# Performance work log

Hardware: AMD Instinct MI355X
Metric: run time of the kernel (lower is better)

Reference implementation:

```python
import jax, jax.numpy as jnp
import numpy as np

N, E, G = 40000, 400000, 64
IN, ED, HID, HEADS, OUT = 2, 18, 64, 4, 3

def _glorot(key, shape):
    fan_in = shape[0]
    return jax.random.normal(key, shape, dtype=jnp.float32) / np.float32(np.sqrt(fan_in))

def setup_inputs():
    key = jax.random.key(0)
    ks = jax.random.split(key, 32)
    d1 = HEADS * HID  # 256
    return {
        "x": jax.random.normal(ks[0], (N, IN), jnp.float32),
        "edge_index": jax.random.randint(ks[1], (2, E), 0, N),
        "edge_attr": jax.random.normal(ks[2], (E, ED), jnp.float32),
        "batch": jnp.sort(jax.random.randint(ks[3], (N,), 0, G)),
        # conv1: TransformerConv(2 -> 64, heads=4, concat=True, beta=True, edge_dim=18)
        "Wq1": _glorot(ks[4], (IN, d1)), "bq1": jnp.zeros((d1,), jnp.float32),
        "Wk1": _glorot(ks[5], (IN, d1)), "bk1": jnp.zeros((d1,), jnp.float32),
        "Wv1": _glorot(ks[6], (IN, d1)), "bv1": jnp.zeros((d1,), jnp.float32),
        "We1": _glorot(ks[7], (ED, d1)),
        "Wskip1": _glorot(ks[8], (IN, d1)), "bskip1": jnp.zeros((d1,), jnp.float32),
        "Wbeta1": _glorot(ks[9], (3 * d1, 1)),
        # conv2: TransformerConv(256 -> 64, heads=1, concat=False, beta=True, edge_dim=18)
        "Wq2": _glorot(ks[10], (d1, HID)), "bq2": jnp.zeros((HID,), jnp.float32),
        "Wk2": _glorot(ks[11], (d1, HID)), "bk2": jnp.zeros((HID,), jnp.float32),
        "Wv2": _glorot(ks[12], (d1, HID)), "bv2": jnp.zeros((HID,), jnp.float32),
        "We2": _glorot(ks[13], (ED, HID)),
        "Wskip2": _glorot(ks[14], (d1, HID)), "bskip2": jnp.zeros((HID,), jnp.float32),
        "Wbeta2": _glorot(ks[15], (3 * HID, 1)),
        "Wlin": _glorot(ks[16], (HID, OUT)), "blin": jnp.zeros((OUT,), jnp.float32),
    }

def _tconv(x, src, dst, edge_attr, Wq, bq, Wk, bk, Wv, bv, We, Wskip, bskip, Wbeta, H, C, concat):
    # PyG TransformerConv with edge_dim, beta=True, root_weight=True (eval: dropout off)
    n = x.shape[0]
    q = (x @ Wq + bq).reshape(n, H, C)
    k = (x @ Wk + bk).reshape(n, H, C)
    v = (x @ Wv + bv).reshape(n, H, C)
    e = (edge_attr @ We).reshape(-1, H, C)              # [E,H,C]
    kj = k[src] + e                                      # key_j + edge
    alpha = jnp.einsum('ehc,ehc->eh', q[dst], kj) * (1.0 / (C ** 0.5))  # [E,H]
    # segment softmax over destination nodes
    amax = jax.ops.segment_max(alpha, dst, num_segments=n)
    ex = jnp.exp(alpha - amax[dst])
    den = jax.ops.segment_sum(ex, dst, num_segments=n)
    w = ex / (den[dst] + 1e-16)
    msg = (v[src] + e) * w[:, :, None]                   # [E,H,C]
    out = jax.ops.segment_sum(msg, dst, num_segments=n)  # [N,H,C]
    out = out.reshape(n, H * C) if concat else out.mean(axis=1)
    # beta-gated skip connection
    xr = x @ Wskip + bskip
    beta = jax.nn.sigmoid(jnp.concatenate([out, xr, out - xr], axis=-1) @ Wbeta)
    return beta * xr + (1.0 - beta) * out

def reference(x, edge_index, edge_attr, batch, Wq1, bq1, Wk1, bk1, Wv1, bv1, We1, Wskip1, bskip1, Wbeta1, Wq2, bq2, Wk2, bk2, Wv2, bv2, We2, Wskip2, bskip2, Wbeta2, Wlin, blin):
    src, dst = edge_index[0], edge_index[1]
    h = jax.nn.relu(_tconv(x, src, dst, edge_attr, Wq1, bq1, Wk1, bk1, Wv1, bv1, We1, Wskip1, bskip1, Wbeta1, HEADS, HID, True))
    h = jax.nn.relu(_tconv(h, src, dst, edge_attr, Wq2, bq2, Wk2, bk2, Wv2, bv2, We2, Wskip2, bskip2, Wbeta2, 1, HID, False))
    # global mean pool per graph
    s = jax.ops.segment_sum(h, batch, num_segments=G)
    cnt = jax.ops.segment_sum(jnp.ones((h.shape[0], 1), h.dtype), batch, num_segments=G)
    pooled = s / jnp.maximum(cnt, 1.0)
    return pooled @ Wlin + blin
```

## Files before the change

### kernel.cpp

```cpp
#include <hip/hip_runtime.h>
#include <hip/hip_fp16.h>

#define N_NODES 40000
#define N_EDGES 400000
#define N_GRAPHS 64
#define D1 256
#define HIDC 64
#define NHEADS 4
#define EDIM 18
#define EPAD 20
#define OUTF 3
#define APAD 264

typedef _Float16 f16x8 __attribute__((ext_vector_type(8)));
typedef float f32x4 __attribute__((ext_vector_type(4)));

__global__ void prep_w(const float* __restrict__ Wq, const float* __restrict__ bq,
                       const float* __restrict__ Wk, const float* __restrict__ bk,
                       const float* __restrict__ Wv, const float* __restrict__ bv,
                       const float* __restrict__ Ws, const float* __restrict__ bs,
                       const float* __restrict__ We2,
                       const float* __restrict__ Wq1, const float* __restrict__ bq1,
                       const float* __restrict__ Wk1, const float* __restrict__ bk1,
                       const float* __restrict__ We1,
                       __half* __restrict__ Bt, float* __restrict__ bias,
                       float* __restrict__ cbuf) {
    int c = blockIdx.x, k = threadIdx.x;
    if (c < 256) {
        int m = c >> 6, d = c & 63;
        const float* W = (m == 0) ? Wq : (m == 1) ? Wk : (m == 2) ? Wv : Ws;
        Bt[c * 256 + k] = __float2half(W[k * 64 + d]);
        if (k == 0) {
            const float* b = (m == 0) ? bq : (m == 1) ? bk : (m == 2) ? bv : bs;
            bias[c] = b[d];
        }
    } else if (c < 288) {
        int j = c - 256;
        float s = 0.f;
        if (j < EDIM)
            for (int cc = 0; cc < 64; ++cc) s += Wq[k * 64 + cc] * We2[j * 64 + cc];
        Bt[c * 256 + k] = __float2half(s);
        if (k == 0) {
            float b = 0.f;
            if (j < EDIM)
                for (int cc = 0; cc < 64; ++cc) b += bq[cc] * We2[j * 64 + cc];
            bias[c] = b;
        }
    } else {
        int t = k;
        if (t < 36) {
            int h = t / 9, r = t % 9, a = r / 3, b = r % 3;
            const float* A = (a == 0) ? Wq1 : (a == 1) ? Wq1 + D1 : bq1;
            const float* B = (b == 0) ? Wk1 : (b == 1) ? Wk1 + D1 : bk1;
            float s = 0.f;
            for (int cc = 0; cc < 64; ++cc) s += A[h * 64 + cc] * B[h * 64 + cc];
            cbuf[h * 63 + a * 3 + b] = s;
        } else if (t < 252) {
            int i = t - 36;
            int h = i / 54, rr = (i % 54) / 18, j = i % 18;
            const float* A = (rr == 0) ? Wq1 : (rr == 1) ? Wq1 + D1 : bq1;
            float s = 0.f;
            for (int cc = 0; cc < 64; ++cc) s += A[h * 64 + cc] * We1[j * D1 + h * 64 + cc];
            cbuf[h * 63 + 9 + rr * 18 + j] = s;
        }
    }
}

__global__ void initA(float* __restrict__ acc1, float* __restrict__ acc2,
                      float* __restrict__ out2, int* __restrict__ deg,
                      float* __restrict__ pooled,
                      int* __restrict__ gs, int* __restrict__ ge) {
    int t = blockIdx.x * 256 + threadIdx.x;
    acc1[t] = 0.f;
    if (t < N_NODES * 64) out2[t] = 0.f;
    if (t < N_NODES * 20) acc2[t] = 0.f;
    if (t < N_NODES) deg[t] = 0;
    if (t < N_GRAPHS * HIDC) pooled[t] = 0.f;
    if (t < N_GRAPHS) { gs[t] = 0; ge[t] = 0; }
}

__global__ void hist_kernel(const int* __restrict__ ei, int* __restrict__ deg,
                            const int* __restrict__ batch, int* __restrict__ gs,
                            int* __restrict__ ge) {
    int e = blockIdx.x * 256 + threadIdx.x;
    if (e < N_EDGES) atomicAdd(&deg[ei[N_EDGES + e]], 1);
    int n = e;
    if (n < N_NODES) {
        int b = batch[n];
        if (n == 0) gs[b] = 0;
        else { int pb = batch[n - 1]; if (pb != b) { ge[pb] = n; gs[b] = n; } }
        if (n == N_NODES - 1) ge[b] = N_NODES;
    }
}

__global__ void scanA(const int* __restrict__ deg, int* __restrict__ bsum) {
    __shared__ int s[256];
    int b = blockIdx.x, t = threadIdx.x;
    s[t] = (t < 160) ? deg[b * 160 + t] : 0;
    __syncthreads();
    for (int off = 128; off; off >>= 1) {
        if (t < off) s[t] += s[t + off];
        __syncthreads();
    }
    if (t == 0) bsum[b] = s[0];
}

__global__ void scanB(const int* __restrict__ bsum, int* __restrict__ boff) {
    __shared__ int s[256];
    int t = threadIdx.x;
    int v = (t < 250) ? bsum[t] : 0;
    s[t] = v;
    __syncthreads();
    for (int off = 1; off < 256; off <<= 1) {
        int add = (t >= off) ? s[t - off] : 0;
        __syncthreads();
        s[t] += add;
        __syncthreads();
    }
    if (t < 250) boff[t] = s[t] - v;
}

__global__ void scanC(const int* __restrict__ deg, const int* __restrict__ boff,
                      int* __restrict__ cursor) {
    __shared__ int s[256];
    int b = blockIdx.x, t = threadIdx.x;
    int v = (t < 160) ? deg[b * 160 + t] : 0;
    s[t] = v;
    __syncthreads();
    for (int off = 1; off < 256; off <<= 1) {
        int add = (t >= off) ? s[t - off] : 0;
        __syncthreads();
        s[t] += add;
        __syncthreads();
    }
    if (t < 160) cursor[b * 160 + t] = boff[b] + s[t] - v;
}

__global__ void scatterE(const int* __restrict__ ei, const float* __restrict__ ea,
                         const float* __restrict__ x, int* __restrict__ cursor,
                         int* __restrict__ src_s, int* __restrict__ dst_s,
                         float* __restrict__ ea_s) {
    int e = blockIdx.x * 256 + threadIdx.x;
    if (e >= N_EDGES) return;
    int src = ei[e], dst = ei[N_EDGES + e];
    const float2* sr = (const float2*)(ea + (size_t)e * EDIM);
    float2 s0 = sr[0], s1 = sr[1], s2 = sr[2], s3 = sr[3], s4 = sr[4],
           s5 = sr[5], s6 = sr[6], s7 = sr[7], s8 = sr[8];
    float2 xv = *(const float2*)(x + (size_t)src * 2);
    int p = atomicAdd(&cursor[dst], 1);
    src_s[p] = src;
    dst_s[p] = dst;
    float4* drow = (float4*)(ea_s + (size_t)p * EPAD);
    drow[0] = make_float4(s0.x, s0.y, s1.x, s1.y);
    drow[1] = make_float4(s2.x, s2.y, s3.x, s3.y);
    drow[2] = make_float4(s4.x, s4.y, s5.x, s5.y);
    drow[3] = make_float4(s6.x, s6.y, s7.x, s7.y);
    drow[4] = make_float4(s8.x, s8.y, xv.x, xv.y);
}

__global__ void logits1(const int* __restrict__ dst_s, const float* __restrict__ ea_s,
                        const float* __restrict__ x, const float* __restrict__ cbuf,
                        float* __restrict__ w1) {
    __shared__ float cb[252];
    int t = threadIdx.x;
    if (t < 252) cb[t] = cbuf[t];
    __syncthreads();
    int p = blockIdx.x * 256 + t;
    if (p >= N_EDGES) return;
    const float4* row = (const float4*)(ea_s + (size_t)p * EPAD);
    float4 r0 = row[0], r1 = row[1], r2 = row[2], r3 = row[3], r4 = row[4];
    float s[EDIM];
    s[0]=r0.x; s[1]=r0.y; s[2]=r0.z; s[3]=r0.w;
    s[4]=r1.x; s[5]=r1.y; s[6]=r1.z; s[7]=r1.w;
    s[8]=r2.x; s[9]=r2.y; s[10]=r2.z; s[11]=r2.w;
    s[12]=r3.x; s[13]=r3.y; s[14]=r3.z; s[15]=r3.w;
    s[16]=r4.x; s[17]=r4.y;
    float xs0 = r4.z, xs1 = r4.w;
    int dst = dst_s[p];
    float2 xd = *(const float2*)(x + (size_t)dst * 2);
    float w[NHEADS];
    #pragma unroll
    for (int h = 0; h < NHEADS; ++h) {
        const float* c = cb + h * 63;
        float alpha = 0.f;
        #pragma unroll
        for (int a = 0; a < 3; ++a) {
            float tv = c[a * 3] * xs0 + c[a * 3 + 1] * xs1 + c[a * 3 + 2];
            const float* cc = c + 9 + a * 18;
            #pragma unroll
            for (int j = 0; j < EDIM; ++j) tv += cc[j] * s[j];
            alpha += tv * ((a == 0) ? xd.x : (a == 1) ? xd.y : 1.f);
        }
        w[h] = __expf(alpha * 0.125f);
    }
    *(float4*)(w1 + (size_t)p * 4) = make_float4(w[0], w[1], w[2], w[3]);
}

__global__ void strip1f(const int* __restrict__ dst_s, const float* __restrict__ ea_s,
                        const float* __restrict__ w1, float* __restrict__ acc1) {
    int t = threadIdx.x;
    int strip = blockIdx.x * 2 + (t >> 7);
    int l = t & 127;
    int h = l >> 5, comp = l & 31;
    bool active = comp < 21;
    int voff = (comp == 0) ? 18 : (comp == 1) ? 19 : (comp >= 3 ? comp - 3 : 0);
    bool isone = (comp == 2);
    int cidx = h * 21 + comp;
    int p0 = strip * 16;
    int dsts[16]; float v[16]; float w[16];
    #pragma unroll
    for (int j = 0; j < 16; ++j) dsts[j] = dst_s[p0 + j];
    #pragma unroll
    for (int j = 0; j < 16; ++j) w[j] = w1[(size_t)(p0 + j) * 4 + h];
    #pragma unroll
    for (int j = 0; j < 16; ++j)
        v[j] = active ? (isone ? 1.f : ea_s[(size_t)(p0 + j) * EPAD + voff]) : 0.f;
    float acc = 0.f;
    int prev = dsts[0];
    #pragma unroll
    for (int j = 0; j < 16; ++j) {
        if (dsts[j] != prev) {
            if (active) atomicAdd(&acc1[(size_t)prev * 84 + cidx], acc);
            acc = 0.f; prev = dsts[j];
        }
        acc += w[j] * v[j];
    }
    if (active) atomicAdd(&acc1[(size_t)prev * 84 + cidx], acc);
}

__global__ void finalize1x(const float* __restrict__ x, const float* __restrict__ acc1,
                           const float* __restrict__ Wv, const float* __restrict__ bv,
                           const float* __restrict__ We, const float* __restrict__ Wskip,
                           const float* __restrict__ bskip, const float* __restrict__ Wbeta,
                           __half* __restrict__ h1f) {
    __shared__ float red[4][4];
    int nb = blockIdx.x * 4;
    int t = threadIdx.x;
    int h = t >> 6;
    float wv0 = Wv[t], wv1 = Wv[D1 + t], bvv = bv[t];
    float we[EDIM];
    #pragma unroll
    for (int j = 0; j < EDIM; ++j) we[j] = We[j * D1 + t];
    float ws0 = Wskip[t], ws1 = Wskip[D1 + t], bsv = bskip[t];
    float wb0 = Wbeta[t], wb1 = Wbeta[D1 + t], wb2 = Wbeta[2 * D1 + t];
    float o[4], xr[4], part[4];
    #pragma unroll
    for (int i = 0; i < 4; ++i) {
        int node = nb + i;
        const float* a = acc1 + (size_t)node * 84 + h * 21;
        float l = a[2];
        float oo = a[0] * wv0 + a[1] * wv1 + l * bvv;
        #pragma unroll
        for (int j = 0; j < EDIM; ++j) oo += a[3 + j] * we[j];
        oo /= (l + 1e-16f);
        float x0 = x[node * 2], x1 = x[node * 2 + 1];
        xr[i] = x0 * ws0 + x1 * ws1 + bsv;
        o[i] = oo;
        part[i] = oo * wb0 + xr[i] * wb1 + (oo - xr[i]) * wb2;
    }
    #pragma unroll
    for (int off = 32; off; off >>= 1) {
        #pragma unroll
        for (int i = 0; i < 4; ++i) part[i] += __shfl_xor(part[i], off);
    }
    if ((t & 63) == 0) {
        #pragma unroll
        for (int i = 0; i < 4; ++i) red[h][i] = part[i];
    }
    __syncthreads();
    #pragma unroll
    for (int i = 0; i < 4; ++i) {
        float tot = red[0][i] + red[1][i] + red[2][i] + red[3][i];
        float beta = 1.f / (1.f + __expf(-tot));
        h1f[(size_t)(nb + i) * D1 + t] =
            __float2half(fmaxf(beta * xr[i] + (1.f - beta) * o[i], 0.f));
    }
}

__device__ __forceinline__ void nl2_store(int c, int gr, float v,
        float* __restrict__ q2, float* __restrict__ k2, __half* __restrict__ v2h,
        float* __restrict__ xr2, float* __restrict__ qe) {
    if (c < 256) {
        int m = c >> 6, d = c & 63;
        if (m == 0)      q2[(size_t)gr * 64 + d] = v;
        else if (m == 1) k2[(size_t)gr * 64 + d] = v;
        else if (m == 2) v2h[(size_t)gr * 64 + d] = __float2half(v);
        else             xr2[(size_t)gr * 64 + d] = v;
    } else {
        qe[(size_t)gr * 32 + (c - 256)] = v;
    }
}

__global__ __launch_bounds__(256) void nl2_mfma(
        const __half* __restrict__ h1f, const __half* __restrict__ Bt,
        const float* __restrict__ bias,
        float* __restrict__ q2, float* __restrict__ k2,
        __half* __restrict__ v2h, float* __restrict__ xr2,
        float* __restrict__ qe) {
    __shared__ _Float16 As[64 * APAD];
    int t = threadIdx.x;
    int row0 = blockIdx.x * 64;
    const float4* gsrc = (const float4*)(h1f + (size_t)row0 * 256);
    #pragma unroll
    for (int i = 0; i < 8; ++i) {
        int li = i * 256 + t;
        int r = li >> 5, c8 = li & 31;
        *(float4*)(As + r * APAD + c8 * 8) = gsrc[li];
    }
    __syncthreads();
    int wave = t >> 6, lane = t & 63, quad = lane >> 4, mm = lane & 15;
    const _Float16* Bp = (const _Float16*)Bt;
    for (int ct = wave; ct < 18; ct += 4) {
        int c0 = ct * 16 + mm;
        const _Float16* b0 = Bp + (size_t)c0 * 256 + quad * 8;
        f16x8 b[8];
        #pragma unroll
        for (int s = 0; s < 8; ++s) b[s] = *(const f16x8*)(b0 + s * 32);
        float bz = bias[c0];
        #pragma unroll
        for (int rt = 0; rt < 4; ++rt) {
            const _Float16* arow = As + (rt * 16 + mm) * APAD + quad * 8;
            f16x8 a[8];
            #pragma unroll
            for (int s = 0; s < 8; ++s) a[s] = *(const f16x8*)(arow + s * 32);
            f32x4 accA = {bz, bz, bz, bz};
            f32x4 accB = {0.f, 0.f, 0.f, 0.f};
            #pragma unroll
            for (int s = 0; s < 4; ++s) {
                accA = __builtin_amdgcn_mfma_f32_16x16x32_f16(a[s],     b[s],     accA, 0, 0, 0);
                accB = __builtin_amdgcn_mfma_f32_16x16x32_f16(a[s + 4], b[s + 4], accB, 0, 0, 0);
            }
            #pragma unroll
            for (int r = 0; r < 4; ++r) {
                int gr = row0 + rt * 16 + quad * 4 + r;
                nl2_store(c0, gr, accA[r] + accB[r], q2, k2, v2h, xr2, qe);
            }
        }
    }
}

#define LG2_BLOCKS 2048
#define LG2_WAVES (LG2_BLOCKS * 4)
__global__ void logits2(const int* __restrict__ src_s, const int* __restrict__ dst_s,
                        const float* __restrict__ ea_s, const float* __restrict__ q2,
                        const float* __restrict__ k2, const float* __restrict__ qe,
                        float* __restrict__ alpha2) {
    int t = threadIdx.x, wid = t >> 6, lane = t & 63;
    int w = blockIdx.x * 4 + wid;
    for (int base = w; base < N_EDGES; base += 2 * LG2_WAVES) {
        int p1 = base, p2 = base + LG2_WAVES;
        bool has2 = p2 < N_EDGES;
        int p2c = has2 ? p2 : p1;
        int s1 = src_s[p1], d1 = dst_s[p1];
        int s2 = src_s[p2c], d2 = dst_s[p2c];
        float dd1 = q2[(size_t)d1 * 64 + lane] * k2[(size_t)s1 * 64 + lane];
        float dd2 = q2[(size_t)d2 * 64 + lane] * k2[(size_t)s2 * 64 + lane];
        if (lane < 20) {
            dd1 += qe[(size_t)d1 * 32 + lane] * ea_s[(size_t)p1 * EPAD + lane];
            dd2 += qe[(size_t)d2 * 32 + lane] * ea_s[(size_t)p2c * EPAD + lane];
        }
        #pragma unroll
        for (int off = 32; off; off >>= 1) {
            dd1 += __shfl_xor(dd1, off);
            dd2 += __shfl_xor(dd2, off);
        }
        if (lane == 0) {
            alpha2[p1] = __expf(dd1 * 0.125f);
            if (has2) alpha2[p2] = __expf(dd2 * 0.125f);
        }
    }
}

__global__ void spmm2s(const int* __restrict__ dst_s, const int* __restrict__ src_s,
                       const float* __restrict__ alpha2, const __half* __restrict__ v2h,
                       const float* __restrict__ ea_s,
                       float* __restrict__ out2, float* __restrict__ acc2) {
    int t = threadIdx.x;
    int strip = blockIdx.x * 4 + (t >> 6);
    int lane = t & 63;
    int p0 = strip * 16;
    int dsts[16]; int srcs[16]; float w[16];
    #pragma unroll
    for (int j = 0; j < 16; ++j) dsts[j] = dst_s[p0 + j];
    #pragma unroll
    for (int j = 0; j < 16; ++j) srcs[j] = src_s[p0 + j];
    #pragma unroll
    for (int j = 0; j < 16; ++j) w[j] = alpha2[p0 + j];
    float vv[16]; float ev[16];
    #pragma unroll
    for (int j = 0; j < 16; ++j) vv[j] = __half2float(v2h[(size_t)srcs[j] * 64 + lane]);
    #pragma unroll
    for (int j = 0; j < 16; ++j)
        ev[j] = (lane < EDIM) ? ea_s[(size_t)(p0 + j) * EPAD + lane] : 1.f;
    float acc = 0.f, accS = 0.f;
    int prev = dsts[0];
    #pragma unroll
    for (int j = 0; j < 16; ++j) {
        if (dsts[j] != prev) {
            atomicAdd(&out2[(size_t)prev * 64 + lane], acc);
            if (lane < 19) atomicAdd(&acc2[(size_t)prev * 20 + lane], accS);
            acc = 0.f; accS = 0.f; prev = dsts[j];
        }
        acc += w[j] * vv[j];
        accS += w[j] * ev[j];
    }
    atomicAdd(&out2[(size_t)prev * 64 + lane], acc);
    if (lane < 19) atomicAdd(&acc2[(size_t)prev * 20 + lane], accS);
}

__global__ void finalize2x(const float* __restrict__ out2, const float* __restrict__ acc2,
                           const float* __restrict__ xr2, const float* __restrict__ We2,
                           const float* __restrict__ Wb2, float* __restrict__ h2) {
    __shared__ float w2s[EDIM * 64];
    int t = threadIdx.x;
    for (int i = t; i < EDIM * 64; i += 256) w2s[i] = We2[i];
    __syncthreads();
    int node = blockIdx.x * 4 + (t >> 6);
    int lane = t & 63;
    const float* a2 = acc2 + (size_t)node * 20;
    float num = out2[(size_t)node * 64 + lane];
    #pragma unroll
    for (int j = 0; j < EDIM; ++j) num += a2[j] * w2s[j * 64 + lane];
    float o = num / (a2[18] + 1e-16f);
    float xr = xr2[(size_t)node * 64 + lane];
    float part = o * Wb2[lane] + xr * Wb2[64 + lane] + (o - xr) * Wb2[128 + lane];
    #pragma unroll
    for (int off = 32; off; off >>= 1) part += __shfl_xor(part, off);
    float beta = 1.f / (1.f + __expf(-part));
    h2[(size_t)node * 64 + lane] = fmaxf(beta * xr + (1.f - beta) * o, 0.f);
}

__global__ void pool_kernel(const float* __restrict__ h2, const int* __restrict__ gs,
                            const int* __restrict__ ge, float* __restrict__ pooled) {
    __shared__ float red[4][64];
    int g = blockIdx.x >> 2, q = blockIdx.x & 3;
    int t = threadIdx.x, wv = t >> 6, lane = t & 63;
    int s = gs[g], e = ge[g];
    float sum = 0.f;
    for (int n = s + q * 4 + wv; n < e; n += 16) sum += h2[(size_t)n * 64 + lane];
    red[wv][lane] = sum;
    __syncthreads();
    if (wv == 0) {
        float v = red[0][lane] + red[1][lane] + red[2][lane] + red[3][lane];
        atomicAdd(&pooled[g * 64 + lane], v);
    }
}

__global__ void final_lin(const float* __restrict__ pooled, const int* __restrict__ gs,
                          const int* __restrict__ ge,
                          const float* __restrict__ Wlin, const float* __restrict__ blin,
                          float* __restrict__ out) {
    int t = threadIdx.x;
    if (t >= N_GRAPHS * OUTF) return;
    int g = t / OUTF, o = t % OUTF;
    int c = ge[g] - gs[g];
    float inv = 1.f / fmaxf((float)c, 1.f);
    float acc = 0.f;
    for (int kk = 0; kk < HIDC; ++kk) acc += pooled[g * 64 + kk] * Wlin[kk * OUTF + o];
    out[t] = acc * inv + blin[o];
}

extern "C" void kernel_launch(void* const* d_in, const int* in_sizes, int n_in,
                              void* d_out, int out_size, void* d_ws, size_t ws_size,
                              hipStream_t stream) {
    const float* x      = (const float*)d_in[0];
    const int*   ei     = (const int*)d_in[1];
    const float* ea     = (const float*)d_in[2];
    const int*   batch  = (const int*)d_in[3];
    const float* Wq1    = (const float*)d_in[4];  const float* bq1    = (const float*)d_in[5];
    const float* Wk1    = (const float*)d_in[6];  const float* bk1    = (const float*)d_in[7];
    const float* Wv1    = (const float*)d_in[8];  const float* bv1    = (const float*)d_in[9];
    const float* We1    = (const float*)d_in[10];
    const float* Wskip1 = (const float*)d_in[11]; const float* bskip1 = (const float*)d_in[12];
    const float* Wbeta1 = (const float*)d_in[13];
    const float* Wq2    = (const float*)d_in[14]; const float* bq2    = (const float*)d_in[15];
    const float* Wk2    = (const float*)d_in[16]; const float* bk2    = (const float*)d_in[17];
    const float* Wv2    = (const float*)d_in[18]; const float* bv2    = (const float*)d_in[19];
    const float* We2    = (const float*)d_in[20];
    const float* Wskip2 = (const float*)d_in[21]; const float* bskip2 = (const float*)d_in[22];
    const float* Wbeta2 = (const float*)d_in[23];
    const float* Wlin   = (const float*)d_in[24]; const float* blin   = (const float*)d_in[25];

    float* ptr = (float*)d_ws;
    float* q2     = ptr; ptr += (size_t)N_NODES * 64;
    float* k2     = ptr; ptr += (size_t)N_NODES * 64;
    float* xr2    = ptr; ptr += (size_t)N_NODES * 64;
    float* qe     = ptr; ptr += (size_t)N_NODES * 32;
    __half* v2h   = (__half*)ptr; ptr += (size_t)N_NODES * 32;
    float* ea_s   = ptr; ptr += (size_t)N_EDGES * EPAD;
    float* alpha2 = ptr; ptr += N_EDGES;
    float* acc2   = ptr; ptr += (size_t)N_NODES * 20;
    float* out2   = ptr; ptr += (size_t)N_NODES * 64;
    float* pooled = ptr; ptr += N_GRAPHS * HIDC;
    int*   gs     = (int*)ptr; ptr += N_GRAPHS;
    int*   ge     = (int*)ptr; ptr += N_GRAPHS;
    float* cbuf   = ptr; ptr += 256;
    float* bias   = ptr; ptr += 320;
    __half* Bt    = (__half*)ptr; ptr += (288 * 256) / 2;
    int*   src_s  = (int*)ptr; ptr += N_EDGES;
    int*   dst_s  = (int*)ptr; ptr += N_EDGES;
    int*   deg    = (int*)ptr; ptr += N_NODES;
    int*   cursor = (int*)ptr; ptr += N_NODES;
    int*   bsum   = (int*)ptr; ptr += 256;
    int*   boff   = (int*)ptr; ptr += 256;
    float* w1     = ptr; ptr += (size_t)N_EDGES * 4;
    float* h2     = ptr; ptr += (size_t)N_NODES * 84;
    float* acc1   = ptr; ptr += (size_t)N_NODES * 84;
    __half* h1f   = (__half*)ptr; ptr += (size_t)N_NODES * 128;

    const int EB = (N_EDGES + 255) / 256;

    prep_w<<<289, 256, 0, stream>>>(Wq2, bq2, Wk2, bk2, Wv2, bv2, Wskip2, bskip2, We2,
                                    Wq1, bq1, Wk1, bk1, We1, Bt, bias, cbuf);
    initA<<<(N_NODES * 84) / 256, 256, 0, stream>>>(acc1, acc2, out2, deg, pooled, gs, ge);
    hist_kernel<<<EB, 256, 0, stream>>>(ei, deg, batch, gs, ge);
    scanA<<<250, 256, 0, stream>>>(deg, bsum);
    scanB<<<1, 256, 0, stream>>>(bsum, boff);
    scanC<<<250, 256, 0, stream>>>(deg, boff, cursor);
    scatterE<<<EB, 256, 0, stream>>>(ei, ea, x, cursor, src_s, dst_s, ea_s);

    logits1<<<EB, 256, 0, stream>>>(dst_s, ea_s, x, cbuf, w1);
    strip1f<<<(N_EDGES / 16) / 2, 256, 0, stream>>>(dst_s, ea_s, w1, acc1);
    finalize1x<<<N_NODES / 4, 256, 0, stream>>>(x, acc1, Wv1, bv1, We1, Wskip1, bskip1,
                                                Wbeta1, h1f);

    nl2_mfma<<<N_NODES / 64, 256, 0, stream>>>(h1f, Bt, bias, q2, k2, v2h, xr2, qe);
    logits2<<<LG2_BLOCKS, 256, 0, stream>>>(src_s, dst_s, ea_s, q2, k2, qe, alpha2);
    spmm2s<<<(N_EDGES / 16) / 4, 256, 0, stream>>>(dst_s, src_s, alpha2, v2h, ea_s,
                                                   out2, acc2);
    finalize2x<<<N_NODES / 4, 256, 0, stream>>>(out2, acc2, xr2, We2, Wbeta2, h2);

    pool_kernel<<<N_GRAPHS * 4, 256, 0, stream>>>(h2, gs, ge, pooled);
    final_lin<<<1, 256, 0, stream>>>(pooled, gs, ge, Wlin, blin, (float*)d_out);
}
```

Baseline: 416.0 us.

## Pack src/dst indices and layer-1 weights into padded per-edge rows

Widens each sorted edge row from 20 to 32 floats so it also carries src, dst and the four layer-1 attention weights. The separate src_s, dst_s and w1 arrays are dropped, and every edge kernel reads one 128-byte row instead of several arrays. acc1 is padded to 96 floats per node with 24 per head, so finalize1x can use float4 loads, and it now handles 16 nodes per block. The cost is more bytes written and read per edge in the sorted buffer, and a larger initA memset.

```diff
diff --git a/kernel.cpp b/kernel.cpp
--- a/kernel.cpp
+++ b/kernel.cpp
@@ -8,7 +8,9 @@
 #define HIDC 64
 #define NHEADS 4
 #define EDIM 18
-#define EPAD 20
+#define EPAD 32
+#define A1PAD 96
+#define NPB1 16
 #define OUTF 3
 #define APAD 264
 
@@ -138,7 +140,6 @@
 
 __global__ void scatterE(const int* __restrict__ ei, const float* __restrict__ ea,
                          const float* __restrict__ x, int* __restrict__ cursor,
-                         int* __restrict__ src_s, int* __restrict__ dst_s,
                          float* __restrict__ ea_s) {
     int e = blockIdx.x * 256 + threadIdx.x;
     if (e >= N_EDGES) return;
@@ -148,27 +149,28 @@
            s5 = sr[5], s6 = sr[6], s7 = sr[7], s8 = sr[8];
     float2 xv = *(const float2*)(x + (size_t)src * 2);
     int p = atomicAdd(&cursor[dst], 1);
-    src_s[p] = src;
-    dst_s[p] = dst;
     float4* drow = (float4*)(ea_s + (size_t)p * EPAD);
     drow[0] = make_float4(s0.x, s0.y, s1.x, s1.y);
     drow[1] = make_float4(s2.x, s2.y, s3.x, s3.y);
     drow[2] = make_float4(s4.x, s4.y, s5.x, s5.y);
     drow[3] = make_float4(s6.x, s6.y, s7.x, s7.y);
     drow[4] = make_float4(s8.x, s8.y, xv.x, xv.y);
-}
-
-__global__ void logits1(const int* __restrict__ dst_s, const float* __restrict__ ea_s,
-                        const float* __restrict__ x, const float* __restrict__ cbuf,
-                        float* __restrict__ w1) {
+    drow[5] = make_float4(__int_as_float(src), __int_as_float(dst), 0.f, 0.f);
+    drow[6] = make_float4(0.f, 0.f, 0.f, 0.f);
+    drow[7] = make_float4(0.f, 0.f, 0.f, 0.f);
+}
+
+__global__ void logits1(float* __restrict__ ea_s, const float* __restrict__ x,
+                        const float* __restrict__ cbuf) {
     __shared__ float cb[252];
     int t = threadIdx.x;
     if (t < 252) cb[t] = cbuf[t];
     __syncthreads();
     int p = blockIdx.x * 256 + t;
     if (p >= N_EDGES) return;
-    const float4* row = (const float4*)(ea_s + (size_t)p * EPAD);
-    float4 r0 = row[0], r1 = row[1], r2 = row[2], r3 = row[3], r4 = row[4];
+    float* rowp = ea_s + (size_t)p * EPAD;
+    const float4* row = (const float4*)rowp;
+    float4 r0 = row[0], r1 = row[1], r2 = row[2], r3 = row[3], r4 = row[4], r5 = row[5];
     float s[EDIM];
     s[0]=r0.x; s[1]=r0.y; s[2]=r0.z; s[3]=r0.w;
     s[4]=r1.x; s[5]=r1.y; s[6]=r1.z; s[7]=r1.w;
@@ -176,7 +178,7 @@
     s[12]=r3.x; s[13]=r3.y; s[14]=r3.z; s[15]=r3.w;
     s[16]=r4.x; s[17]=r4.y;
     float xs0 = r4.z, xs1 = r4.w;
-    int dst = dst_s[p];
+    int dst = __float_as_int(r5.y);
     float2 xd = *(const float2*)(x + (size_t)dst * 2);
     float w[NHEADS];
     #pragma unroll
@@ -193,11 +195,10 @@
         }
         w[h] = __expf(alpha * 0.125f);
     }
-    *(float4*)(w1 + (size_t)p * 4) = make_float4(w[0], w[1], w[2], w[3]);
-}
-
-__global__ void strip1f(const int* __restrict__ dst_s, const float* __restrict__ ea_s,
-                        const float* __restrict__ w1, float* __restrict__ acc1) {
+    *(float4*)(rowp + 24) = make_float4(w[0], w[1], w[2], w[3]);
+}
+
+__global__ void strip1f(const float* __restrict__ ea_s, float* __restrict__ acc1) {
     int t = threadIdx.x;
     int strip = blockIdx.x * 2 + (t >> 7);
     int l = t & 127;
@@ -205,13 +206,14 @@
     bool active = comp < 21;
     int voff = (comp == 0) ? 18 : (comp == 1) ? 19 : (comp >= 3 ? comp - 3 : 0);
     bool isone = (comp == 2);
-    int cidx = h * 21 + comp;
+    int cidx = h * 24 + comp;
     int p0 = strip * 16;
     int dsts[16]; float v[16]; float w[16];
     #pragma unroll
-    for (int j = 0; j < 16; ++j) dsts[j] = dst_s[p0 + j];
-    #pragma unroll
-    for (int j = 0; j < 16; ++j) w[j] = w1[(size_t)(p0 + j) * 4 + h];
+    for (int j = 0; j < 16; ++j)
+        dsts[j] = __float_as_int(ea_s[(size_t)(p0 + j) * EPAD + 21]);
+    #pragma unroll
+    for (int j = 0; j < 16; ++j) w[j] = ea_s[(size_t)(p0 + j) * EPAD + 24 + h];
     #pragma unroll
     for (int j = 0; j < 16; ++j)
         v[j] = active ? (isone ? 1.f : ea_s[(size_t)(p0 + j) * EPAD + voff]) : 0.f;
@@ -220,12 +222,12 @@
     #pragma unroll
     for (int j = 0; j < 16; ++j) {
         if (dsts[j] != prev) {
-            if (active) atomicAdd(&acc1[(size_t)prev * 84 + cidx], acc);
+            if (active) atomicAdd(&acc1[(size_t)prev * A1PAD + cidx], acc);
             acc = 0.f; prev = dsts[j];
         }
         acc += w[j] * v[j];
     }
-    if (active) atomicAdd(&acc1[(size_t)prev * 84 + cidx], acc);
+    if (active) atomicAdd(&acc1[(size_t)prev * A1PAD + cidx], acc);
 }
 
 __global__ void finalize1x(const float* __restrict__ x, const float* __restrict__ acc1,
@@ -233,8 +235,8 @@
                            const float* __restrict__ We, const float* __restrict__ Wskip,
                            const float* __restrict__ bskip, const float* __restrict__ Wbeta,
                            __half* __restrict__ h1f) {
-    __shared__ float red[4][4];
-    int nb = blockIdx.x * 4;
+    __shared__ float red[4][NPB1];
+    int nb = blockIdx.x * NPB1;
     int t = threadIdx.x;
     int h = t >> 6;
     float wv0 = Wv[t], wv1 = Wv[D1 + t], bvv = bv[t];
@@ -243,37 +245,44 @@
     for (int j = 0; j < EDIM; ++j) we[j] = We[j * D1 + t];
     float ws0 = Wskip[t], ws1 = Wskip[D1 + t], bsv = bskip[t];
     float wb0 = Wbeta[t], wb1 = Wbeta[D1 + t], wb2 = Wbeta[2 * D1 + t];
-    float o[4], xr[4], part[4];
-    #pragma unroll
-    for (int i = 0; i < 4; ++i) {
-        int node = nb + i;
-        const float* a = acc1 + (size_t)node * 84 + h * 21;
-        float l = a[2];
-        float oo = a[0] * wv0 + a[1] * wv1 + l * bvv;
-        #pragma unroll
-        for (int j = 0; j < EDIM; ++j) oo += a[3 + j] * we[j];
-        oo /= (l + 1e-16f);
-        float x0 = x[node * 2], x1 = x[node * 2 + 1];
-        xr[i] = x0 * ws0 + x1 * ws1 + bsv;
-        o[i] = oo;
-        part[i] = oo * wb0 + xr[i] * wb1 + (oo - xr[i]) * wb2;
-    }
-    #pragma unroll
-    for (int off = 32; off; off >>= 1) {
-        #pragma unroll
-        for (int i = 0; i < 4; ++i) part[i] += __shfl_xor(part[i], off);
-    }
-    if ((t & 63) == 0) {
-        #pragma unroll
-        for (int i = 0; i < 4; ++i) red[h][i] = part[i];
-    }
-    __syncthreads();
-    #pragma unroll
-    for (int i = 0; i < 4; ++i) {
-        float tot = red[0][i] + red[1][i] + red[2][i] + red[3][i];
-        float beta = 1.f / (1.f + __expf(-tot));
-        h1f[(size_t)(nb + i) * D1 + t] =
-            __float2half(fmaxf(beta * xr[i] + (1.f - beta) * o[i], 0.f));
+    for (int i0 = 0; i0 < NPB1; i0 += 4) {
+        float o[4], xr[4], part[4];
+        #pragma unroll
+        for (int i = 0; i < 4; ++i) {
+            int node = nb + i0 + i;
+            const float4* a4 = (const float4*)(acc1 + (size_t)node * A1PAD + h * 24);
+            float4 q0 = a4[0], q1 = a4[1], q2v = a4[2], q3 = a4[3], q4 = a4[4], q5 = a4[5];
+            float l = q0.z;
+            float oo = q0.x * wv0 + q0.y * wv1 + l * bvv;
+            oo += q0.w * we[0];
+            oo += q1.x * we[1] + q1.y * we[2] + q1.z * we[3] + q1.w * we[4];
+            oo += q2v.x * we[5] + q2v.y * we[6] + q2v.z * we[7] + q2v.w * we[8];
+            oo += q3.x * we[9] + q3.y * we[10] + q3.z * we[11] + q3.w * we[12];
+            oo += q4.x * we[13] + q4.y * we[14] + q4.z * we[15] + q4.w * we[16];
+            oo += q5.x * we[17];
+            oo /= (l + 1e-16f);
+            float x0 = x[node * 2], x1 = x[node * 2 + 1];
+            xr[i] = x0 * ws0 + x1 * ws1 + bsv;
+            o[i] = oo;
+            part[i] = oo * wb0 + xr[i] * wb1 + (oo - xr[i]) * wb2;
+        }
+        #pragma unroll
+        for (int off = 32; off; off >>= 1) {
+            #pragma unroll
+            for (int i = 0; i < 4; ++i) part[i] += __shfl_xor(part[i], off);
+        }
+        if ((t & 63) == 0) {
+            #pragma unroll
+            for (int i = 0; i < 4; ++i) red[h][i0 + i] = part[i];
+        }
+        __syncthreads();
+        #pragma unroll
+        for (int i = 0; i < 4; ++i) {
+            float tot = red[0][i0 + i] + red[1][i0 + i] + red[2][i0 + i] + red[3][i0 + i];
+            float beta = 1.f / (1.f + __expf(-tot));
+            h1f[(size_t)(nb + i0 + i) * D1 + t] =
+                __float2half(fmaxf(beta * xr[i] + (1.f - beta) * o[i], 0.f));
+        }
     }
 }
 
@@ -341,8 +350,7 @@
 
 #define LG2_BLOCKS 2048
 #define LG2_WAVES (LG2_BLOCKS * 4)
-__global__ void logits2(const int* __restrict__ src_s, const int* __restrict__ dst_s,
-                        const float* __restrict__ ea_s, const float* __restrict__ q2,
+__global__ void logits2(const float* __restrict__ ea_s, const float* __restrict__ q2,
                         const float* __restrict__ k2, const float* __restrict__ qe,
                         float* __restrict__ alpha2) {
     int t = threadIdx.x, wid = t >> 6, lane = t & 63;
@@ -351,13 +359,15 @@
         int p1 = base, p2 = base + LG2_WAVES;
         bool has2 = p2 < N_EDGES;
         int p2c = has2 ? p2 : p1;
-        int s1 = src_s[p1], d1 = dst_s[p1];
-        int s2 = src_s[p2c], d2 = dst_s[p2c];
+        const float* row1 = ea_s + (size_t)p1 * EPAD;
+        const float* row2 = ea_s + (size_t)p2c * EPAD;
+        int s1 = __float_as_int(row1[20]), d1 = __float_as_int(row1[21]);
+        int s2 = __float_as_int(row2[20]), d2 = __float_as_int(row2[21]);
         float dd1 = q2[(size_t)d1 * 64 + lane] * k2[(size_t)s1 * 64 + lane];
         float dd2 = q2[(size_t)d2 * 64 + lane] * k2[(size_t)s2 * 64 + lane];
         if (lane < 20) {
-            dd1 += qe[(size_t)d1 * 32 + lane] * ea_s[(size_t)p1 * EPAD + lane];
-            dd2 += qe[(size_t)d2 * 32 + lane] * ea_s[(size_t)p2c * EPAD + lane];
+            dd1 += qe[(size_t)d1 * 32 + lane] * row1[lane];
+            dd2 += qe[(size_t)d2 * 32 + lane] * row2[lane];
         }
         #pragma unroll
         for (int off = 32; off; off >>= 1) {
@@ -371,9 +381,8 @@
     }
 }
 
-__global__ void spmm2s(const int* __restrict__ dst_s, const int* __restrict__ src_s,
+__global__ void spmm2s(const float* __restrict__ ea_s,
                        const float* __restrict__ alpha2, const __half* __restrict__ v2h,
-                       const float* __restrict__ ea_s,
                        float* __restrict__ out2, float* __restrict__ acc2) {
     int t = threadIdx.x;
     int strip = blockIdx.x * 4 + (t >> 6);
@@ -381,9 +390,11 @@
     int p0 = strip * 16;
     int dsts[16]; int srcs[16]; float w[16];
     #pragma unroll
-    for (int j = 0; j < 16; ++j) dsts[j] = dst_s[p0 + j];
-    #pragma unroll
-    for (int j = 0; j < 16; ++j) srcs[j] = src_s[p0 + j];
+    for (int j = 0; j < 16; ++j)
+        dsts[j] = __float_as_int(ea_s[(size_t)(p0 + j) * EPAD + 21]);
+    #pragma unroll
+    for (int j = 0; j < 16; ++j)
+        srcs[j] = __float_as_int(ea_s[(size_t)(p0 + j) * EPAD + 20]);
     #pragma unroll
     for (int j = 0; j < 16; ++j) w[j] = alpha2[p0 + j];
     float vv[16]; float ev[16];
@@ -497,37 +508,34 @@
     float* cbuf   = ptr; ptr += 256;
     float* bias   = ptr; ptr += 320;
     __half* Bt    = (__half*)ptr; ptr += (288 * 256) / 2;
-    int*   src_s  = (int*)ptr; ptr += N_EDGES;
-    int*   dst_s  = (int*)ptr; ptr += N_EDGES;
     int*   deg    = (int*)ptr; ptr += N_NODES;
     int*   cursor = (int*)ptr; ptr += N_NODES;
     int*   bsum   = (int*)ptr; ptr += 256;
     int*   boff   = (int*)ptr; ptr += 256;
-    float* w1     = ptr; ptr += (size_t)N_EDGES * 4;
-    float* h2     = ptr; ptr += (size_t)N_NODES * 84;
-    float* acc1   = ptr; ptr += (size_t)N_NODES * 84;
+    float* h2     = ptr; ptr += (size_t)N_NODES * 64;
+    float* acc1   = ptr; ptr += (size_t)N_NODES * A1PAD;
     __half* h1f   = (__half*)ptr; ptr += (size_t)N_NODES * 128;
 
     const int EB = (N_EDGES + 255) / 256;
 
     prep_w<<<289, 256, 0, stream>>>(Wq2, bq2, Wk2, bk2, Wv2, bv2, Wskip2, bskip2, We2,
                                     Wq1, bq1, Wk1, bk1, We1, Bt, bias, cbuf);
-    initA<<<(N_NODES * 84) / 256, 256, 0, stream>>>(acc1, acc2, out2, deg, pooled, gs, ge);
+    initA<<<(N_NODES * A1PAD) / 256, 256, 0, stream>>>(acc1, acc2, out2, deg, pooled,
+                                                       gs, ge);
     hist_kernel<<<EB, 256, 0, stream>>>(ei, deg, batch, gs, ge);
     scanA<<<250, 256, 0, stream>>>(deg, bsum);
     scanB<<<1, 256, 0, stream>>>(bsum, boff);
     scanC<<<250, 256, 0, stream>>>(deg, boff, cursor);
-    scatterE<<<EB, 256, 0, stream>>>(ei, ea, x, cursor, src_s, dst_s, ea_s);
-
-    logits1<<<EB, 256, 0, stream>>>(dst_s, ea_s, x, cbuf, w1);
-    strip1f<<<(N_EDGES / 16) / 2, 256, 0, stream>>>(dst_s, ea_s, w1, acc1);
-    finalize1x<<<N_NODES / 4, 256, 0, stream>>>(x, acc1, Wv1, bv1, We1, Wskip1, bskip1,
-                                                Wbeta1, h1f);
+    scatterE<<<EB, 256, 0, stream>>>(ei, ea, x, cursor, ea_s);
+
+    logits1<<<EB, 256, 0, stream>>>(ea_s, x, cbuf);
+    strip1f<<<(N_EDGES / 16) / 2, 256, 0, stream>>>(ea_s, acc1);
+    finalize1x<<<N_NODES / NPB1, 256, 0, stream>>>(x, acc1, Wv1, bv1, We1, Wskip1, bskip1,
+                                                   Wbeta1, h1f);
 
     nl2_mfma<<<N_NODES / 64, 256, 0, stream>>>(h1f, Bt, bias, q2, k2, v2h, xr2, qe);
-    logits2<<<LG2_BLOCKS, 256, 0, stream>>>(src_s, dst_s, ea_s, q2, k2, qe, alpha2);
-    spmm2s<<<(N_EDGES / 16) / 4, 256, 0, stream>>>(dst_s, src_s, alpha2, v2h, ea_s,
-                                                   out2, acc2);
+    logits2<<<LG2_BLOCKS, 256, 0, stream>>>(ea_s, q2, k2, qe, alpha2);
+    spmm2s<<<(N_EDGES / 16) / 4, 256, 0, stream>>>(ea_s, alpha2, v2h, out2, acc2);
     finalize2x<<<N_NODES / 4, 256, 0, stream>>>(out2, acc2, xr2, We2, Wbeta2, h2);
 
     pool_kernel<<<N_GRAPHS * 4, 256, 0, stream>>>(h2, gs, ge, pooled);
```

Measured after the change: 429.5 us. 1.03x slower.

## Replace LDS-staged node GEMM with register-resident A fragments per wave

Applied to the files above, without the earlier changes.

The layer-2 node projection GEMM no longer stages a 64-row tile of h1 in shared memory. Each wave now loads one 16-row A fragment straight into registers and computes 6 of the 18 output column tiles, so three waves share each row tile. This removes the LDS round trip and the block barrier and raises the number of blocks. In exchange, A rows are read from global memory three times and each B column tile is reused over fewer rows.

```diff
diff --git a/kernel.cpp b/kernel.cpp
--- a/kernel.cpp
+++ b/kernel.cpp
@@ -10,7 +10,6 @@
 #define EDIM 18
 #define EPAD 20
 #define OUTF 3
-#define APAD 264
 
 typedef _Float16 f16x8 __attribute__((ext_vector_type(8)));
 typedef float f32x4 __attribute__((ext_vector_type(4)));
@@ -291,50 +290,42 @@
     }
 }
 
-__global__ __launch_bounds__(256) void nl2_mfma(
+__global__ __launch_bounds__(256) void nl2_reg(
         const __half* __restrict__ h1f, const __half* __restrict__ Bt,
         const float* __restrict__ bias,
         float* __restrict__ q2, float* __restrict__ k2,
         __half* __restrict__ v2h, float* __restrict__ xr2,
         float* __restrict__ qe) {
-    __shared__ _Float16 As[64 * APAD];
-    int t = threadIdx.x;
-    int row0 = blockIdx.x * 64;
-    const float4* gsrc = (const float4*)(h1f + (size_t)row0 * 256);
-    #pragma unroll
-    for (int i = 0; i < 8; ++i) {
-        int li = i * 256 + t;
-        int r = li >> 5, c8 = li & 31;
-        *(float4*)(As + r * APAD + c8 * 8) = gsrc[li];
-    }
-    __syncthreads();
-    int wave = t >> 6, lane = t & 63, quad = lane >> 4, mm = lane & 15;
+    int t = threadIdx.x;
+    int w = blockIdx.x * 4 + (t >> 6);
+    int lane = t & 63, quad = lane >> 4, mm = lane & 15;
+    int rt = w / 3, cg = w % 3;
+    int row0 = rt * 16;
+    const _Float16* ap = (const _Float16*)h1f + (size_t)(row0 + mm) * 256 + quad * 8;
+    f16x8 a[8];
+    #pragma unroll
+    for (int s = 0; s < 8; ++s) a[s] = *(const f16x8*)(ap + s * 32);
     const _Float16* Bp = (const _Float16*)Bt;
-    for (int ct = wave; ct < 18; ct += 4) {
+    #pragma unroll
+    for (int ci = 0; ci < 6; ++ci) {
+        int ct = cg * 6 + ci;
         int c0 = ct * 16 + mm;
         const _Float16* b0 = Bp + (size_t)c0 * 256 + quad * 8;
         f16x8 b[8];
         #pragma unroll
         for (int s = 0; s < 8; ++s) b[s] = *(const f16x8*)(b0 + s * 32);
         float bz = bias[c0];
-        #pragma unroll
-        for (int rt = 0; rt < 4; ++rt) {
-            const _Float16* arow = As + (rt * 16 + mm) * APAD + quad * 8;
-            f16x8 a[8];
-            #pragma unroll
-            for (int s = 0; s < 8; ++s) a[s] = *(const f16x8*)(arow + s * 32);
-            f32x4 accA = {bz, bz, bz, bz};
-            f32x4 accB = {0.f, 0.f, 0.f, 0.f};
-            #pragma unroll
-            for (int s = 0; s < 4; ++s) {
-                accA = __builtin_amdgcn_mfma_f32_16x16x32_f16(a[s],     b[s],     accA, 0, 0, 0);
-                accB = __builtin_amdgcn_mfma_f32_16x16x32_f16(a[s + 4], b[s + 4], accB, 0, 0, 0);
-            }
-            #pragma unroll
-            for (int r = 0; r < 4; ++r) {
-                int gr = row0 + rt * 16 + quad * 4 + r;
-                nl2_store(c0, gr, accA[r] + accB[r], q2, k2, v2h, xr2, qe);
-            }
+        f32x4 accA = {bz, bz, bz, bz};
+        f32x4 accB = {0.f, 0.f, 0.f, 0.f};
+        #pragma unroll
+        for (int s = 0; s < 4; ++s) {
+            accA = __builtin_amdgcn_mfma_f32_16x16x32_f16(a[s],     b[s],     accA, 0, 0, 0);
+            accB = __builtin_amdgcn_mfma_f32_16x16x32_f16(a[s + 4], b[s + 4], accB, 0, 0, 0);
+        }
+        #pragma unroll
+        for (int r = 0; r < 4; ++r) {
+            int gr = row0 + quad * 4 + r;
+            nl2_store(c0, gr, accA[r] + accB[r], q2, k2, v2h, xr2, qe);
         }
     }
 }
@@ -524,7 +515,8 @@
     finalize1x<<<N_NODES / 4, 256, 0, stream>>>(x, acc1, Wv1, bv1, We1, Wskip1, bskip1,
                                                 Wbeta1, h1f);
 
-    nl2_mfma<<<N_NODES / 64, 256, 0, stream>>>(h1f, Bt, bias, q2, k2, v2h, xr2, qe);
+    nl2_reg<<<(N_NODES / 16) * 3 / 4, 256, 0, stream>>>(h1f, Bt, bias, q2, k2, v2h,
+                                                        xr2, qe);
     logits2<<<LG2_BLOCKS, 256, 0, stream>>>(src_s, dst_s, ea_s, q2, k2, qe, alpha2);
     spmm2s<<<(N_EDGES / 16) / 4, 256, 0, stream>>>(dst_s, src_s, alpha2, v2h, ea_s,
                                                    out2, acc2);
```

Measured after the change: 424.4 us. 1.02x slower.
